# Optimization experiments

Hardware: AMD Instinct MI355X
Metric: run time of the kernel (lower is better)

## Reference

```python
import jax, jax.numpy as jnp
import numpy as np

NH = NW = 16           # superpixel grid (num_spixels = 256 = 16*16)
NSPIX = NH * NW
N_ITERS = 5


def setup_inputs() -> dict:
    key = jax.random.key(0)
    B, C, H, W = 4, 64, 512, 512
    return {"f": jax.random.normal(key, (B, C, H, W), dtype=jnp.float32)}


def _neighbor_tables(h, w):
    # nearest-neighbor upsampled initial label map (torch F.interpolate 'nearest')
    row = jnp.arange(h) * NH // h
    col = jnp.arange(w) * NW // w
    init_label = (row[:, None] * NW + col[None, :]).reshape(-1)     # [P]
    init_row = init_label // NW
    init_col = init_label % NW
    idxs, valids = [], []
    # offset order matches torch: cat([r-NW, r, r+NW]) with r=[-1,0,1]
    for k in range(9):
        dr, dc = k // 3 - 1, k % 3 - 1
        r, c = init_row + dr, init_col + dc
        valid = (r >= 0) & (r < NH) & (c >= 0) & (c < NW)
        idxs.append(jnp.where(valid, r * NW + c, 0))
        valids.append(valid)
    return init_label, jnp.stack(idxs), jnp.stack(valids)            # [9,P], [9,P]


def _ssn_forward(f):
    b, c, h, w = f.shape
    P = h * w
    # adaptive_avg_pool2d to (NH,NW): plain block mean since h%NH==0, w%NW==0
    spix = f.reshape(b, c, NH, h // NH, NW, w // NW).mean(axis=(3, 5))
    spix = spix.reshape(b, c, NSPIX).transpose(0, 2, 1)              # [B,S,C]
    feats = f.reshape(b, c, P).transpose(0, 2, 1)                    # [B,P,C]
    _, nb_idx, nb_valid = _neighbor_tables(h, w)

    seg_sum = jax.vmap(lambda v, s: jax.ops.segment_sum(v, s, num_segments=NSPIX),
                       in_axes=(0, None))

    affinity = None
    for _ in range(N_ITERS):
        # pixel -> 9 candidate-center squared distances
        dists = []
        for k in range(9):
            g = spix[:, nb_idx[k], :]                                # [B,P,C] gather
            d2 = ((feats - g) ** 2).sum(-1)                          # [B,P]
            dists.append(jnp.where(nb_valid[k][None], d2, jnp.inf))
        dist = jnp.stack(dists, axis=1)                              # [B,9,P]
        affinity = jax.nn.softmax(-dist, axis=1)                     # [B,9,P]
        # scatter-add weighted features into centers
        numer = jnp.zeros((b, NSPIX, c), f.dtype)
        denom = jnp.zeros((b, NSPIX), f.dtype)
        for k in range(9):
            wgt = affinity[:, k]                                     # [B,P]
            numer = numer + seg_sum(wgt[..., None] * feats, nb_idx[k])
            denom = denom + seg_sum(wgt, nb_idx[k])
        spix = numer / (denom[..., None] + 1e-16)                    # [B,S,C]

    rel = jnp.argmax(affinity, axis=1)                               # [B,P]
    hard_labels = nb_idx[rel, jnp.arange(P)[None, :]].astype(jnp.int32)
    return spix, hard_labels


def reference(f):
    # returns (spixel_features [B, nspix, C], hard_labels [B, H*W])
    return _ssn_forward(f)
```

## Files before the change

kernel.cpp:

```cpp
#include <hip/hip_runtime.h>
#include <hip/hip_bf16.h>
#include <cstdint>
#include <cstddef>

#define CH    64
#define IMG   512
#define PLANE (IMG * IMG)
#define NSPX  256

__global__ __launch_bounds__(64) void ssn_pool(const float* __restrict__ f,
                                               float* __restrict__ numer,
                                               float* __restrict__ denom) {
  const int wg = blockIdx.x;
  const int b = wg >> 8, sp = wg & 255;
  const int sr = sp >> 4, sc = sp & 15;
  const int c = threadIdx.x;
  const int y0 = sr * 32, x0 = sc * 32;
  const float* base = f + (size_t)(b * CH + c) * PLANE;
  float acc = 0.f;
  for (int y = 0; y < 32; ++y) {
    const float4* rp = (const float4*)(base + (size_t)(y0 + y) * IMG + x0);
    #pragma unroll
    for (int xv = 0; xv < 8; ++xv) {
      float4 v = rp[xv];
      acc = __fadd_rn(acc, v.x);
      acc = __fadd_rn(acc, v.y);
      acc = __fadd_rn(acc, v.z);
      acc = __fadd_rn(acc, v.w);
    }
  }
  numer[((size_t)wg << 6) + c] = acc;
  if (c == 0) denom[wg] = 1024.0f;
}

__global__ __launch_bounds__(256, 3) void ssn_iter2(const float* __restrict__ f,
    const float* __restrict__ numer_in, const float* __restrict__ denom_in,
    float* __restrict__ Pnum, float* __restrict__ Pden,
    float* __restrict__ labels_out, const int final_flag) {
  const int wg = blockIdx.x;
  const int b = wg >> 8, sp = wg & 255;
  const int sr = sp >> 4, sc = sp & 15;
  const int tid = threadIdx.x;
  const int wave = tid >> 6, lane = tid & 63;
  const int p = lane & 31, h = lane >> 5;

  __shared__ float cent[9][64];
  __shared__ float nw[4][9][64];
  __shared__ float dw[4][9];
  __shared__ int   nbr_s[9];
  __shared__ __align__(16) float v_lds[4][32][65];
  __shared__ __align__(16) float w_lds[4][32][12];

  if (tid < 9) {
    int dr = tid / 3 - 1, dc = tid % 3 - 1;
    int nr = sr + dr, nc = sc + dc;
    bool valid = (nr >= 0) && (nr < 16) && (nc >= 0) && (nc < 16);
    nbr_s[tid] = valid ? (nr * 16 + nc) : -1;
  }
  __syncthreads();
  for (int i = tid; i < 9 * 64; i += 256) {
    int k = i >> 6, c = i & 63;
    int ns = nbr_s[k];
    float v = 0.f;
    if (ns >= 0) {
      int base = (b << 8) + ns;
      v = numer_in[((size_t)base << 6) + c] / (denom_in[base] + 1e-16f);
    }
    cent[k][c] = v;
  }
  __syncthreads();

  int nbk[9];
  #pragma unroll
  for (int k = 0; k < 9; ++k) nbk[k] = nbr_s[k];

  float nacc[9], wsA[9];
  #pragma unroll
  for (int k = 0; k < 9; ++k) { nacc[k] = 0.f; wsA[k] = 0.f; }

  const int y0 = sr * 32, x0 = sc * 32;
  float (* __restrict__ vb)[65] = v_lds[wave];
  float (* __restrict__ wb)[12] = w_lds[wave];

  const int cbase = lane >> 3;
  const int xq    = (lane & 7) * 4;

  for (int r = 0; r < 8; ++r) {
    const int gy = y0 + wave * 8 + r;

    #pragma unroll
    for (int j = 0; j < 8; ++j) {
      const int c = j * 8 + cbase;
      const float4 v4 = *(const float4*)(
          f + (size_t)(b * CH + c) * PLANE + (size_t)gy * IMG + x0 + xq);
      vb[xq + 0][c] = v4.x;
      vb[xq + 1][c] = v4.y;
      vb[xq + 2][c] = v4.z;
      vb[xq + 3][c] = v4.w;
    }
    __builtin_amdgcn_wave_barrier();

    float dpart[9];
    #pragma unroll
    for (int k = 0; k < 9; ++k) dpart[k] = 0.f;
    #pragma unroll
    for (int cit = 0; cit < 32; ++cit) {
      float v = vb[p][32 * h + cit];
      #pragma unroll
      for (int k = 0; k < 9; ++k) {
        float d = v - cent[k][32 * h + cit];
        dpart[k] = fmaf(d, d, dpart[k]);
      }
    }
    float dist[9];
    #pragma unroll
    for (int k = 0; k < 9; ++k) {
      float o = __shfl_xor(dpart[k], 32);
      dist[k] = (nbk[k] >= 0) ? (dpart[k] + o) : __builtin_inff();
    }
    float m = dist[0];
    #pragma unroll
    for (int k = 1; k < 9; ++k) m = fminf(m, dist[k]);
    float w[9], s = 0.f;
    #pragma unroll
    for (int k = 0; k < 9; ++k) { w[k] = expf(m - dist[k]); s = __fadd_rn(s, w[k]); }
    #pragma unroll
    for (int k = 0; k < 9; ++k) w[k] = w[k] / s;

    if (final_flag) {
      float ba = w[0]; int bs = nbk[0];
      #pragma unroll
      for (int k = 1; k < 9; ++k)
        if (w[k] > ba) { ba = w[k]; bs = nbk[k]; }
      if (h == 0)
        labels_out[(size_t)b * PLANE + (size_t)gy * IMG + x0 + p] = (float)bs;
    }

    if (h == 0) {
      *(float4*)&wb[p][0] = make_float4(w[0], w[1], w[2], w[3]);
      *(float4*)&wb[p][4] = make_float4(w[4], w[5], w[6], w[7]);
      wb[p][8] = w[8];
    }

    #pragma unroll 8
    for (int pp = 0; pp < 32; ++pp) {
      float v  = vb[pp][lane];
      float4 wA = *(const float4*)&wb[pp][0];
      float4 wB = *(const float4*)&wb[pp][4];
      float  w8 = wb[pp][8];
      nacc[0] = __fadd_rn(nacc[0], __fmul_rn(wA.x, v));
      nacc[1] = __fadd_rn(nacc[1], __fmul_rn(wA.y, v));
      nacc[2] = __fadd_rn(nacc[2], __fmul_rn(wA.z, v));
      nacc[3] = __fadd_rn(nacc[3], __fmul_rn(wA.w, v));
      nacc[4] = __fadd_rn(nacc[4], __fmul_rn(wB.x, v));
      nacc[5] = __fadd_rn(nacc[5], __fmul_rn(wB.y, v));
      nacc[6] = __fadd_rn(nacc[6], __fmul_rn(wB.z, v));
      nacc[7] = __fadd_rn(nacc[7], __fmul_rn(wB.w, v));
      nacc[8] = __fadd_rn(nacc[8], __fmul_rn(w8,  v));
      wsA[0] = __fadd_rn(wsA[0], wA.x);
      wsA[1] = __fadd_rn(wsA[1], wA.y);
      wsA[2] = __fadd_rn(wsA[2], wA.z);
      wsA[3] = __fadd_rn(wsA[3], wA.w);
      wsA[4] = __fadd_rn(wsA[4], wB.x);
      wsA[5] = __fadd_rn(wsA[5], wB.y);
      wsA[6] = __fadd_rn(wsA[6], wB.z);
      wsA[7] = __fadd_rn(wsA[7], wB.w);
      wsA[8] = __fadd_rn(wsA[8], w8);
    }
    __builtin_amdgcn_wave_barrier();
  }

  #pragma unroll
  for (int k = 0; k < 9; ++k) nw[wave][k][lane] = nacc[k];
  if (lane == 0) {
    #pragma unroll
    for (int k = 0; k < 9; ++k) dw[wave][k] = wsA[k];
  }
  __syncthreads();

  for (int i = tid; i < 9 * 64; i += 256) {
    int k = i >> 6, c = i & 63;
    float s01  = __fadd_rn(nw[0][k][c], nw[1][k][c]);
    float s012 = __fadd_rn(s01, nw[2][k][c]);
    Pnum[((size_t)wg * 9 + k) * 64 + c] = __fadd_rn(s012, nw[3][k][c]);
  }
  if (tid < 9) {
    float s01  = __fadd_rn(dw[0][tid], dw[1][tid]);
    float s012 = __fadd_rn(s01, dw[2][tid]);
    Pden[wg * 9 + tid] = __fadd_rn(s012, dw[3][tid]);
  }
}

__global__ __launch_bounds__(64) void ssn_gather(const float* __restrict__ Pnum,
    const float* __restrict__ Pden, float* __restrict__ numer_out,
    float* __restrict__ denom_out, float* __restrict__ spix_out,
    const int final_mode) {
  const int wg = blockIdx.x;
  const int b = wg >> 8, sp = wg & 255;
  const int sr = sp >> 4, sc = sp & 15;
  const int c = threadIdx.x;
  float acc = 0.f, den = 0.f;
  #pragma unroll
  for (int k = 0; k < 9; ++k) {
    int dr = k / 3 - 1, dc = k % 3 - 1;
    int ssr = sr - dr, ssc = sc - dc;
    if (ssr >= 0 && ssr < 16 && ssc >= 0 && ssc < 16) {
      int src = (b << 8) + ssr * 16 + ssc;
      acc = __fadd_rn(acc, Pnum[((size_t)src * 9 + k) * 64 + c]);
      den = __fadd_rn(den, Pden[src * 9 + k]);
    }
  }
  if (final_mode) {
    spix_out[((size_t)wg << 6) + c] = acc / (den + 1e-16f);
  } else {
    numer_out[((size_t)wg << 6) + c] = acc;
    if (c == 0) denom_out[wg] = den;
  }
}

extern "C" void kernel_launch(void* const* d_in, const int* in_sizes, int n_in,
                              void* d_out, int out_size, void* d_ws, size_t ws_size,
                              hipStream_t stream) {
  const float* f = (const float*)d_in[0];
  float* out = (float*)d_out;
  float* ws  = (float*)d_ws;
  float* labels = out + 4 * NSPX * CH;

  float* Pnum   = ws;
  float* Pden   = ws + 589824;
  float* numerA = ws + 599040;
  float* numerB = ws + 664576;
  float* denomA = ws + 730112;
  float* denomB = ws + 731136;

  ssn_pool<<<dim3(1024), dim3(64), 0, stream>>>(f, numerA, denomA);

  float* ni = numerA; float* di = denomA;
  float* no = numerB; float* dn = denomB;
  for (int it = 0; it < 5; ++it) {
    ssn_iter2<<<dim3(1024), dim3(256), 0, stream>>>(f, ni, di, Pnum, Pden, labels,
                                                    (it == 4) ? 1 : 0);
    if (it < 4) {
      ssn_gather<<<dim3(1024), dim3(64), 0, stream>>>(Pnum, Pden, no, dn, nullptr, 0);
      float* t;
      t = ni; ni = no; no = t;
      t = di; di = dn; dn = t;
    } else {
      ssn_gather<<<dim3(1024), dim3(64), 0, stream>>>(Pnum, Pden, nullptr, nullptr, out, 1);
    }
  }
}
```

Baseline: 810.8 us.

## Software-prefetch next pixel row into registers in pool and iteration kernels

Both the pooling kernel and the per-iteration kernel now load the next image row's float4 values into registers while the current row is processed from LDS, double-buffering global loads against compute. The pooling kernel is also restructured so each lane loads coalesced 32-pixel rows across channels and transposes through LDS, where before each lane walked one channel plane. This is meant to hide global memory latency. It raises register pressure by 32 extra floats per thread, which under the 256x3 launch bound may spill or lower occupancy.

```diff
diff --git a/kernel.cpp b/kernel.cpp
--- a/kernel.cpp
+++ b/kernel.cpp
@@ -8,29 +8,57 @@
 #define PLANE (IMG * IMG)
 #define NSPX  256
 
-__global__ __launch_bounds__(64) void ssn_pool(const float* __restrict__ f,
-                                               float* __restrict__ numer,
-                                               float* __restrict__ denom) {
+__global__ __launch_bounds__(64) void ssn_pool2(const float* __restrict__ f,
+                                                float* __restrict__ numer,
+                                                float* __restrict__ denom) {
   const int wg = blockIdx.x;
   const int b = wg >> 8, sp = wg & 255;
   const int sr = sp >> 4, sc = sp & 15;
-  const int c = threadIdx.x;
+  const int lane = threadIdx.x;
   const int y0 = sr * 32, x0 = sc * 32;
-  const float* base = f + (size_t)(b * CH + c) * PLANE;
+  const int cbase = lane >> 3;
+  const int xq    = (lane & 7) * 4;
+
+  __shared__ __align__(16) float vb[32][65];
+
+  const float* fB = f + (size_t)b * CH * PLANE;
+
+  float4 cur[8], nxt[8];
+  #pragma unroll
+  for (int j = 0; j < 8; ++j) {
+    const int c = j * 8 + cbase;
+    cur[j] = *(const float4*)(fB + (size_t)c * PLANE + (size_t)y0 * IMG + x0 + xq);
+  }
+
   float acc = 0.f;
   for (int y = 0; y < 32; ++y) {
-    const float4* rp = (const float4*)(base + (size_t)(y0 + y) * IMG + x0);
-    #pragma unroll
-    for (int xv = 0; xv < 8; ++xv) {
-      float4 v = rp[xv];
-      acc = __fadd_rn(acc, v.x);
-      acc = __fadd_rn(acc, v.y);
-      acc = __fadd_rn(acc, v.z);
-      acc = __fadd_rn(acc, v.w);
-    }
-  }
-  numer[((size_t)wg << 6) + c] = acc;
-  if (c == 0) denom[wg] = 1024.0f;
+    if (y < 31) {
+      #pragma unroll
+      for (int j = 0; j < 8; ++j) {
+        const int c = j * 8 + cbase;
+        nxt[j] = *(const float4*)(fB + (size_t)c * PLANE +
+                                  (size_t)(y0 + y + 1) * IMG + x0 + xq);
+      }
+    }
+    #pragma unroll
+    for (int j = 0; j < 8; ++j) {
+      const int c = j * 8 + cbase;
+      vb[xq + 0][c] = cur[j].x;
+      vb[xq + 1][c] = cur[j].y;
+      vb[xq + 2][c] = cur[j].z;
+      vb[xq + 3][c] = cur[j].w;
+    }
+    __builtin_amdgcn_wave_barrier();
+    #pragma unroll 8
+    for (int x = 0; x < 32; ++x) acc = __fadd_rn(acc, vb[x][lane]);
+    __builtin_amdgcn_wave_barrier();
+    if (y < 31) {
+      #pragma unroll
+      for (int j = 0; j < 8; ++j) cur[j] = nxt[j];
+    }
+  }
+  numer[((size_t)wg << 6) + lane] = acc;
+  if (lane == 0) denom[wg] = 1024.0f;
 }
 
 __global__ __launch_bounds__(256, 3) void ssn_iter2(const float* __restrict__ f,
@@ -84,19 +112,36 @@
 
   const int cbase = lane >> 3;
   const int xq    = (lane & 7) * 4;
+  const float* fRow = f + (size_t)b * CH * PLANE + (size_t)x0 + xq;
+
+  float4 cur[8], nxt[8];
+  {
+    const int gy = y0 + wave * 8;
+    #pragma unroll
+    for (int j = 0; j < 8; ++j) {
+      const int c = j * 8 + cbase;
+      cur[j] = *(const float4*)(fRow + (size_t)c * PLANE + (size_t)gy * IMG);
+    }
+  }
 
   for (int r = 0; r < 8; ++r) {
     const int gy = y0 + wave * 8 + r;
 
+    if (r < 7) {
+      #pragma unroll
+      for (int j = 0; j < 8; ++j) {
+        const int c = j * 8 + cbase;
+        nxt[j] = *(const float4*)(fRow + (size_t)c * PLANE + (size_t)(gy + 1) * IMG);
+      }
+    }
+
     #pragma unroll
     for (int j = 0; j < 8; ++j) {
       const int c = j * 8 + cbase;
-      const float4 v4 = *(const float4*)(
-          f + (size_t)(b * CH + c) * PLANE + (size_t)gy * IMG + x0 + xq);
-      vb[xq + 0][c] = v4.x;
-      vb[xq + 1][c] = v4.y;
-      vb[xq + 2][c] = v4.z;
-      vb[xq + 3][c] = v4.w;
+      vb[xq + 0][c] = cur[j].x;
+      vb[xq + 1][c] = cur[j].y;
+      vb[xq + 2][c] = cur[j].z;
+      vb[xq + 3][c] = cur[j].w;
     }
     __builtin_amdgcn_wave_barrier();
 
@@ -168,6 +213,11 @@
       wsA[8] = __fadd_rn(wsA[8], w8);
     }
     __builtin_amdgcn_wave_barrier();
+
+    if (r < 7) {
+      #pragma unroll
+      for (int j = 0; j < 8; ++j) cur[j] = nxt[j];
+    }
   }
 
   #pragma unroll
@@ -233,7 +283,7 @@
   float* denomA = ws + 730112;
   float* denomB = ws + 731136;
 
-  ssn_pool<<<dim3(1024), dim3(64), 0, stream>>>(f, numerA, denomA);
+  ssn_pool2<<<dim3(1024), dim3(64), 0, stream>>>(f, numerA, denomA);
 
   float* ni = numerA; float* di = denomA;
   float* no = numerB; float* dn = denomB;
```

After: 921.8 us. +13.7%, slower.
